# Optimization experiments

Measured on AMD Instinct MI355X. Metric: run time of the kernel, lower is better.

## Reference

```python
import jax, jax.numpy as jnp
import numpy as np

N_HEADS = 8
D_EMBED = 512
D_HEAD = D_EMBED // N_HEADS


def setup_inputs() -> dict:
    key = jax.random.key(0)
    ks = jax.random.split(key, 5)
    x = jax.random.normal(ks[0], (1, 4096, D_EMBED), dtype=jnp.float32)
    # in_proj: Linear(d, 3d); out_proj: Linear(d, d). Stored as [in, out] for x @ W.
    scale_in = 1.0 / np.sqrt(D_EMBED)
    W_in = jax.random.uniform(ks[1], (D_EMBED, 3 * D_EMBED), jnp.float32, -scale_in, scale_in)
    b_in = jax.random.uniform(ks[2], (3 * D_EMBED,), jnp.float32, -scale_in, scale_in)
    W_out = jax.random.uniform(ks[3], (D_EMBED, D_EMBED), jnp.float32, -scale_in, scale_in)
    b_out = jax.random.uniform(ks[4], (D_EMBED,), jnp.float32, -scale_in, scale_in)
    return {"x": x, "W_in": W_in, "b_in": b_in, "W_out": W_out, "b_out": b_out,
            "causal_mask": 1}


def reference(x, W_in, b_in, W_out, b_out, causal_mask):
    B, S, D = x.shape
    qkv = x @ W_in + b_in                      # [B, S, 3D]
    q, k, v = jnp.split(qkv, 3, axis=-1)
    # [B, S, D] -> [B, H, S, d_head]
    def split_heads(t):
        return t.reshape(B, S, N_HEADS, D_HEAD).transpose(0, 2, 1, 3)
    q, k, v = split_heads(q), split_heads(k), split_heads(v)
    weight = jnp.einsum("bhqd,bhkd->bhqk", q, k)  # [B, H, S, S]
    if causal_mask:
        mask = jnp.triu(jnp.ones((S, S), dtype=bool), k=1)
        weight = jnp.where(mask, -jnp.inf, weight)
    weight = weight / jnp.sqrt(jnp.float32(D_HEAD)).astype(weight.dtype)
    weight = jax.nn.softmax(weight, axis=-1)
    out = jnp.einsum("bhqk,bhkd->bhqd", weight, v)  # [B, H, S, d_head]
    out = out.transpose(0, 2, 1, 3).reshape(B, S, D)
    return out @ W_out + b_out
```

## Files before the change

### kernel.cpp

```cpp
#include <hip/hip_runtime.h>
#include <math.h>

#define SEQ 4096
#define DM 512
#define NH 8
#define DH 64
#define TQK (3 * DM)
#define QSCALE 0.18033688011112042f

typedef __attribute__((ext_vector_type(8))) short bf16x8;
typedef __attribute__((ext_vector_type(4))) float floatx4;
typedef unsigned short ushort_t;

__device__ __forceinline__ floatx4 mfma16(bf16x8 a, bf16x8 b, floatx4 c) {
    return __builtin_amdgcn_mfma_f32_16x16x32_bf16(a, b, c, 0, 0, 0);
}
__device__ __forceinline__ float ex2(float x) { return __builtin_amdgcn_exp2f(x); }

__device__ __forceinline__ unsigned int pk2(float a, float b) {
    unsigned int ua = __float_as_uint(a); ua = (ua + 0x7FFFu + ((ua >> 16) & 1u)) >> 16;
    unsigned int ub = __float_as_uint(b); ub = (ub + 0x7FFFu + ((ub >> 16) & 1u)) >> 16;
    return ua | (ub << 16);
}
__device__ __forceinline__ unsigned short f2bf(float x) {
    unsigned int u = __float_as_uint(x);
    return (unsigned short)((u + 0x7FFFu + ((u >> 16) & 1u)) >> 16);
}
__device__ __forceinline__ float bflo(unsigned int u) { return __uint_as_float(u << 16); }
__device__ __forceinline__ float bfhi(unsigned int u) { return __uint_as_float(u & 0xFFFF0000u); }

__device__ __forceinline__ void gload_lds16(const void* g, void* l) {
    __builtin_amdgcn_global_load_lds(
        (const __attribute__((address_space(1))) unsigned int*)g,
        (__attribute__((address_space(3))) unsigned int*)l, 16, 0, 0);
}

#define DPPMAX(x, ctrl) \
    (x) = fmaxf((x), __int_as_float(__builtin_amdgcn_update_dpp(0, __float_as_int(x), (ctrl), 0xF, 0xF, true)))
__device__ __forceinline__ float row_max16(float x) {
    DPPMAX(x, 0xB1);
    DPPMAX(x, 0x4E);
    DPPMAX(x, 0x141);
    DPPMAX(x, 0x140);
    return x;
}

__global__ __launch_bounds__(256) void prep(const float* __restrict__ x,
                                            const float* __restrict__ W_in,
                                            const float* __restrict__ W_out,
                                            ushort_t* __restrict__ xb,
                                            ushort_t* __restrict__ wti,
                                            ushort_t* __restrict__ wto) {
    __shared__ float T[64][65];
    const int bid = blockIdx.x, tid = threadIdx.x;
    if (bid < 1024) {
        const int i = bid * 256 + tid;
        const float4* p = (const float4*)x + (size_t)i * 2;
        float4 f0 = p[0], f1 = p[1];
        ((uint4*)xb)[i] = make_uint4(pk2(f0.x, f0.y), pk2(f0.z, f0.w),
                                     pk2(f1.x, f1.y), pk2(f1.z, f1.w));
        return;
    }
    const float* W; ushort_t* WT; int N, K, n0, k0; bool qscale;
    if (bid < 1216) { int id = bid - 1024; W = W_in;  WT = wti; N = TQK; K = DM;
                      n0 = (id % 24) * 64; k0 = (id / 24) * 64; qscale = true; }
    else            { int id = bid - 1216; W = W_out; WT = wto; N = DM;  K = DM;
                      n0 = (id % 8) * 64;  k0 = (id / 8) * 64;  qscale = false; }
    {
        const int r = tid >> 2, g = tid & 3;
        const float* src = W + (size_t)(k0 + r) * N + n0 + g * 16;
#pragma unroll
        for (int i = 0; i < 4; i++) {
            float4 f = ((const float4*)src)[i];
            T[g * 16 + i * 4 + 0][r] = f.x;
            T[g * 16 + i * 4 + 1][r] = f.y;
            T[g * 16 + i * 4 + 2][r] = f.z;
            T[g * 16 + i * 4 + 3][r] = f.w;
        }
    }
    __syncthreads();
    const int nr = tid >> 2, g2 = tid & 3;
    const float sc = (qscale && (n0 + nr < DM)) ? QSCALE : 1.0f;
    unsigned int pk[8];
#pragma unroll
    for (int j = 0; j < 8; j++)
        pk[j] = pk2(T[nr][g2 * 16 + 2 * j] * sc, T[nr][g2 * 16 + 2 * j + 1] * sc);
    ushort_t* dst = WT + (size_t)(n0 + nr) * K + k0 + g2 * 16;
    ((uint4*)dst)[0] = make_uint4(pk[0], pk[1], pk[2], pk[3]);
    ((uint4*)dst)[1] = make_uint4(pk[4], pk[5], pk[6], pk[7]);
}

__global__ __launch_bounds__(256) void gemm_in(const ushort_t* __restrict__ A,
                                               const ushort_t* __restrict__ BT,
                                               const float* __restrict__ bias,
                                               ushort_t* __restrict__ Cv,
                                               ushort_t* __restrict__ vt_out) {
    __shared__ __align__(16) ushort_t As[2][128 * 64];
    __shared__ __align__(16) ushort_t Bs[2][128 * 64];
    const int tid  = threadIdx.x;
    const int lane = tid & 63;
    const int w    = tid >> 6;
    const int quad = lane >> 4;
    const int ln   = lane & 15;
    const int row0 = blockIdx.y * 128;
    const int col0 = blockIdx.x * 128;
    const int wm = w >> 1, wn = w & 1;
    const int srow = lane >> 3;
    const int js   = (lane & 7) ^ srow;
    const int K = DM, N = TQK;

    floatx4 acc[4][4];
#pragma unroll
    for (int i = 0; i < 4; i++)
#pragma unroll
        for (int j = 0; j < 4; j++) acc[i][j] = (floatx4){0.f, 0.f, 0.f, 0.f};

#pragma unroll
    for (int i = 0; i < 4; i++) {
        const int c = w * 4 + i;
        gload_lds16(A  + (size_t)(row0 + c * 8 + srow) * K + js * 8, &As[0][c * 512]);
        gload_lds16(BT + (size_t)(col0 + c * 8 + srow) * K + js * 8, &Bs[0][c * 512]);
    }

    for (int kt = 0; kt < 8; kt++) {
        const int cur = kt & 1;
        __syncthreads();
        if (kt < 7) {
            const int k0n = (kt + 1) << 6;
#pragma unroll
            for (int i = 0; i < 4; i++) {
                const int c = w * 4 + i;
                gload_lds16(A  + (size_t)(row0 + c * 8 + srow) * K + k0n + js * 8, &As[cur ^ 1][c * 512]);
                gload_lds16(BT + (size_t)(col0 + c * 8 + srow) * K + k0n + js * 8, &Bs[cur ^ 1][c * 512]);
            }
        }
#pragma unroll
        for (int s = 0; s < 2; s++) {
            bf16x8 af[4], bfr[4];
#pragma unroll
            for (int i = 0; i < 4; i++) {
                const int lm = wm * 64 + i * 16 + ln;
                af[i] = *(const bf16x8*)&As[cur][lm * 64 + ((s * 4 + quad) ^ (ln & 7)) * 8];
                const int lnn = wn * 64 + i * 16 + ln;
                bfr[i] = *(const bf16x8*)&Bs[cur][lnn * 64 + ((s * 4 + quad) ^ (ln & 7)) * 8];
            }
#pragma unroll
            for (int i = 0; i < 4; i++)
#pragma unroll
                for (int j = 0; j < 4; j++)
                    acc[i][j] = mfma16(af[i], bfr[j], acc[i][j]);
        }
    }

    if (col0 >= 2 * DM) {
#pragma unroll
        for (int j = 0; j < 4; j++) {
            const int n = col0 + wn * 64 + j * 16 + ln;
            const float bv = bias[n];
#pragma unroll
            for (int i = 0; i < 4; i++) {
                const int mb = row0 + wm * 64 + i * 16 + quad * 4;
                uint2 pkd;
                pkd.x = pk2(acc[i][j][0] + bv, acc[i][j][1] + bv);
                pkd.y = pk2(acc[i][j][2] + bv, acc[i][j][3] + bv);
                *(uint2*)&vt_out[(size_t)(n - 2 * DM) * SEQ + mb] = pkd;
            }
        }
        return;
    }

#pragma unroll
    for (int j = 0; j < 4; j++) {
        const int n = col0 + wn * 64 + j * 16 + ln;
        const float bv = bias[n] * ((n < DM) ? QSCALE : 1.0f);
#pragma unroll
        for (int i = 0; i < 4; i++) {
            const int mb = row0 + wm * 64 + i * 16 + quad * 4;
#pragma unroll
            for (int r = 0; r < 4; r++)
                Cv[(size_t)(mb + r) * N + n] = f2bf(acc[i][j][r] + bv);
        }
    }
}

__global__ __launch_bounds__(256, 3) void attn_split(const ushort_t* __restrict__ qkv_b,
                                                     const ushort_t* __restrict__ vt,
                                                     ushort_t* __restrict__ po,
                                                     float2* __restrict__ pml) {
    __shared__ __align__(16) ushort_t Ks[2][64 * 64];
    __shared__ __align__(16) ushort_t Vs[2][64 * 64];
    __shared__ __align__(16) ushort_t Ps[128 * 72];

    const int tid  = threadIdx.x;
    const int lane = tid & 63;
    const int w    = tid >> 6;
    const int quad = lane >> 4;
    const int ln   = lane & 15;
    const int h    = blockIdx.y;
    const int lnx7 = ln & 7;

    const int e = 143 - (int)blockIdx.x;
    int g = 0;
    while (e >= 2 * (g + 1) * (g + 2)) g++;
    const int off = e - 2 * g * (g + 1);
    const int nc  = g + 1;
    const int qt  = 4 * g + off / nc;
    const int c   = off % nc;
    const int T   = 2 * qt + 2;
    const int jt0 = (c * T) / nc;
    const int jt1 = ((c + 1) * T) / nc;
    const int q0  = qt * 128;

    bf16x8 a0[2], a1[2];
#pragma unroll
    for (int qg = 0; qg < 2; qg++) {
        const ushort_t* qrow = qkv_b + (size_t)(q0 + w * 32 + qg * 16 + ln) * TQK + h * DH;
        a0[qg] = *(const bf16x8*)(qrow + quad * 8);
        a1[qg] = *(const bf16x8*)(qrow + quad * 8 + 32);
    }

    const short oneb = (short)0x3F80;
    const bf16x8 vone = {oneb, oneb, oneb, oneb, oneb, oneb, oneb, oneb};

    float m_q[2] = {-INFINITY, -INFINITY};
    floatx4 o[2][4], ol[2];
#pragma unroll
    for (int qg = 0; qg < 2; qg++) {
#pragma unroll
        for (int t = 0; t < 4; t++) o[qg][t] = (floatx4){0.f, 0.f, 0.f, 0.f};
        ol[qg] = (floatx4){0.f, 0.f, 0.f, 0.f};
    }

    const int srow = lane >> 3;
    const int js   = (lane & 7) ^ srow;

    {
        const int k0 = jt0 * 64;
#pragma unroll
        for (int i = 0; i < 2; i++) {
            const int cg = w * 2 + i;
            gload_lds16(qkv_b + (size_t)(k0 + cg * 8 + srow) * TQK + DM + h * DH + js * 8,
                        &Ks[0][cg * 512]);
            gload_lds16(vt + (size_t)(h * DH + cg * 8 + srow) * SEQ + k0 + js * 8,
                        &Vs[0][cg * 512]);
        }
    }

    for (int jt = jt0; jt < jt1; ++jt) {
        const int cur = (jt - jt0) & 1;
        const int k0  = jt * 64;
        __syncthreads();
        if (jt + 1 < jt1) {
            const int k0n = (jt + 1) * 64;
#pragma unroll
            for (int i = 0; i < 2; i++) {
                const int cg = w * 2 + i;
                gload_lds16(qkv_b + (size_t)(k0n + cg * 8 + srow) * TQK + DM + h * DH + js * 8,
                            &Ks[cur ^ 1][cg * 512]);
                gload_lds16(vt + (size_t)(h * DH + cg * 8 + srow) * SEQ + k0n + js * 8,
                            &Vs[cur ^ 1][cg * 512]);
            }
        }

        bf16x8 kb0[4], kb1[4];
#pragma unroll
        for (int t = 0; t < 4; t++) {
            const int n = t * 16 + ln;
            kb0[t] = *(const bf16x8*)&Ks[cur][n * 64 + ((quad) ^ lnx7) * 8];
            kb1[t] = *(const bf16x8*)&Ks[cur][n * 64 + ((4 + quad) ^ lnx7) * 8];
        }

#pragma unroll
        for (int qg = 0; qg < 2; qg++) {
            floatx4 sa[4];
#pragma unroll
            for (int t = 0; t < 4; t++) {
                floatx4 acc = {0.f, 0.f, 0.f, 0.f};
                acc = mfma16(a0[qg], kb0[t], acc);
                acc = mfma16(a1[qg], kb1[t], acc);
                sa[t] = acc;
            }

            if (k0 + 63 > q0 + w * 32 + qg * 16) {
#pragma unroll
                for (int t = 0; t < 4; t++) {
                    const int cg2 = k0 + t * 16 + ln;
#pragma unroll
                    for (int r = 0; r < 4; r++) {
                        const int rg = q0 + w * 32 + qg * 16 + quad * 4 + r;
                        if (cg2 > rg) sa[t][r] = -INFINITY;
                    }
                }
            }

            float mx = sa[0][0];
#pragma unroll
            for (int t = 0; t < 4; t++)
#pragma unroll
                for (int r = 0; r < 4; r++) mx = fmaxf(mx, sa[t][r]);
            mx = row_max16(mx);
            const float mn = fmaxf(fmaxf(m_q[qg], mx), -1e30f);
            const float alpha = ex2(m_q[qg] - mn);
            m_q[qg] = mn;
#pragma unroll
            for (int t = 0; t < 4; t++)
#pragma unroll
                for (int r = 0; r < 4; r++) {
                    const float p = ex2(sa[t][r] - mn);
                    Ps[(w * 32 + qg * 16 + quad * 4 + r) * 72 + t * 16 + ln] =
                        (ushort_t)(__float_as_uint(p) >> 16);
                }
            if (alpha < 1.0f) {
#pragma unroll
                for (int t = 0; t < 4; t++)
#pragma unroll
                    for (int r = 0; r < 4; r++) o[qg][t][r] *= alpha;
#pragma unroll
                for (int r = 0; r < 4; r++) ol[qg][r] *= alpha;
            }
        }

        __builtin_amdgcn_wave_barrier();

#pragma unroll
        for (int t = 0; t < 4; t++) {
            const int d = t * 16 + ln;
            const bf16x8 v0 = *(const bf16x8*)&Vs[cur][d * 64 + ((quad) ^ lnx7) * 8];
            const bf16x8 v1 = *(const bf16x8*)&Vs[cur][d * 64 + ((4 + quad) ^ lnx7) * 8];
#pragma unroll
            for (int qg = 0; qg < 2; qg++) {
                const bf16x8 p0 = *(const bf16x8*)&Ps[(w * 32 + qg * 16 + ln) * 72 + quad * 8];
                const bf16x8 p1 = *(const bf16x8*)&Ps[(w * 32 + qg * 16 + ln) * 72 + quad * 8 + 32];
                o[qg][t] = mfma16(p0, v0, o[qg][t]);
                o[qg][t] = mfma16(p1, v1, o[qg][t]);
                if (t == 0) {
                    ol[qg] = mfma16(p0, vone, ol[qg]);
                    ol[qg] = mfma16(p1, vone, ol[qg]);
                }
            }
        }
    }

    const size_t pbase  = ((size_t)h * 144 + e) * (128 * 64);
    const size_t mlbase = ((size_t)h * 144 + e) * 128;
#pragma unroll
    for (int qg = 0; qg < 2; qg++) {
#pragma unroll
        for (int t = 0; t < 4; t++)
#pragma unroll
            for (int r = 0; r < 4; r++)
                po[pbase + (size_t)(w * 32 + qg * 16 + quad * 4 + r) * 64 + t * 16 + ln] =
                    f2bf(o[qg][t][r]);
        if (ln == 0) {
#pragma unroll
            for (int r = 0; r < 4; r++)
                pml[mlbase + w * 32 + qg * 16 + quad * 4 + r] = make_float2(m_q[qg], ol[qg][r]);
        }
    }
}

__global__ __launch_bounds__(512) void attn_combine(const ushort_t* __restrict__ po,
                                                    const float2* __restrict__ pml,
                                                    ushort_t* __restrict__ aob) {
    const int qt = blockIdx.x, h = blockIdx.y;
    const int gq = qt >> 2;
    const int nc = gq + 1;
    const int sbase = 2 * gq * (gq + 1) + (qt & 3) * nc;
    const int row = threadIdx.x >> 2, g = threadIdx.x & 3;

    float2 ml[8];
    float M = -INFINITY;
    for (int ci = 0; ci < nc; ci++) {
        ml[ci] = pml[((size_t)h * 144 + sbase + ci) * 128 + row];
        M = fmaxf(M, ml[ci].x);
    }
    float L = 0.f;
    float acc[16];
#pragma unroll
    for (int j = 0; j < 16; j++) acc[j] = 0.f;

    for (int ci = 0; ci < nc; ci++) {
        const float wgt = ex2(ml[ci].x - M);
        L += wgt * ml[ci].y;
        const ushort_t* p = po + ((size_t)h * 144 + sbase + ci) * (128 * 64)
                               + (size_t)row * 64 + g * 16;
        uint4 u0 = ((const uint4*)p)[0];
        uint4 u1 = ((const uint4*)p)[1];
        const unsigned int uu[8] = {u0.x, u0.y, u0.z, u0.w, u1.x, u1.y, u1.z, u1.w};
#pragma unroll
        for (int j = 0; j < 8; j++) {
            acc[2 * j]     += wgt * bflo(uu[j]);
            acc[2 * j + 1] += wgt * bfhi(uu[j]);
        }
    }
    const float inv = 1.0f / L;
    unsigned int pk[8];
#pragma unroll
    for (int j = 0; j < 8; j++)
        pk[j] = pk2(acc[2 * j] * inv, acc[2 * j + 1] * inv);
    ushort_t* dst = aob + (size_t)(qt * 128 + row) * DM + h * DH + g * 16;
    ((uint4*)dst)[0] = make_uint4(pk[0], pk[1], pk[2], pk[3]);
    ((uint4*)dst)[1] = make_uint4(pk[4], pk[5], pk[6], pk[7]);
}

__global__ __launch_bounds__(256) void gemm_out(const ushort_t* __restrict__ A,
                                                const ushort_t* __restrict__ BT,
                                                const float* __restrict__ bias,
                                                float* __restrict__ out) {
    __shared__ __align__(16) ushort_t As[2][128 * 64];
    __shared__ __align__(16) ushort_t Bs[2][64 * 64];
    const int tid  = threadIdx.x;
    const int lane = tid & 63;
    const int w    = tid >> 6;
    const int quad = lane >> 4;
    const int ln   = lane & 15;
    const int row0 = blockIdx.y * 128;
    const int col0 = blockIdx.x * 64;
    const int wm = w >> 1, wn = w & 1;
    const int srow = lane >> 3;
    const int js   = (lane & 7) ^ srow;

    floatx4 acc[4][2];
#pragma unroll
    for (int i = 0; i < 4; i++)
#pragma unroll
        for (int j = 0; j < 2; j++) acc[i][j] = (floatx4){0.f, 0.f, 0.f, 0.f};

#pragma unroll
    for (int i = 0; i < 4; i++) {
        const int c = w * 4 + i;
        gload_lds16(A + (size_t)(row0 + c * 8 + srow) * DM + js * 8, &As[0][c * 512]);
    }
#pragma unroll
    for (int i = 0; i < 2; i++) {
        const int c = w * 2 + i;
        gload_lds16(BT + (size_t)(col0 + c * 8 + srow) * DM + js * 8, &Bs[0][c * 512]);
    }

    for (int kt = 0; kt < 8; kt++) {
        const int cur = kt & 1;
        __syncthreads();
        if (kt < 7) {
            const int k0n = (kt + 1) << 6;
#pragma unroll
            for (int i = 0; i < 4; i++) {
                const int c = w * 4 + i;
                gload_lds16(A + (size_t)(row0 + c * 8 + srow) * DM + k0n + js * 8, &As[cur ^ 1][c * 512]);
            }
#pragma unroll
            for (int i = 0; i < 2; i++) {
                const int c = w * 2 + i;
                gload_lds16(BT + (size_t)(col0 + c * 8 + srow) * DM + k0n + js * 8, &Bs[cur ^ 1][c * 512]);
            }
        }
#pragma unroll
        for (int s = 0; s < 2; s++) {
            bf16x8 af[4], bfr[2];
#pragma unroll
            for (int i = 0; i < 4; i++) {
                const int lm = wm * 64 + i * 16 + ln;
                af[i] = *(const bf16x8*)&As[cur][lm * 64 + ((s * 4 + quad) ^ (ln & 7)) * 8];
            }
#pragma unroll
            for (int j = 0; j < 2; j++) {
                const int lnn = wn * 32 + j * 16 + ln;
                bfr[j] = *(const bf16x8*)&Bs[cur][lnn * 64 + ((s * 4 + quad) ^ (ln & 7)) * 8];
            }
#pragma unroll
            for (int i = 0; i < 4; i++)
#pragma unroll
                for (int j = 0; j < 2; j++)
                    acc[i][j] = mfma16(af[i], bfr[j], acc[i][j]);
        }
    }

#pragma unroll
    for (int j = 0; j < 2; j++) {
        const int n = col0 + wn * 32 + j * 16 + ln;
        const float bv = bias[n];
#pragma unroll
        for (int i = 0; i < 4; i++) {
            const int mb = row0 + wm * 64 + i * 16 + quad * 4;
#pragma unroll
            for (int r = 0; r < 4; r++)
                out[(size_t)(mb + r) * DM + n] = acc[i][j][r] + bv;
        }
    }
}

extern "C" void kernel_launch(void* const* d_in, const int* in_sizes, int n_in,
                              void* d_out, int out_size, void* d_ws, size_t ws_size,
                              hipStream_t stream) {
    const float* x     = (const float*)d_in[0];
    const float* W_in  = (const float*)d_in[1];
    const float* b_in  = (const float*)d_in[2];
    const float* W_out = (const float*)d_in[3];
    const float* b_out = (const float*)d_in[4];
    float* out = (float*)d_out;

    char* ws = (char*)d_ws;
    ushort_t* xb    = (ushort_t*)ws;
    ushort_t* wti   = (ushort_t*)(ws + (4u  << 20));
    ushort_t* wto   = (ushort_t*)(ws + (6u  << 20));
    ushort_t* qkv_b = (ushort_t*)(ws + (7u  << 20));
    ushort_t* vtb   = (ushort_t*)(ws + (19u << 20));
    ushort_t* po    = (ushort_t*)(ws + (23u << 20));
    float2*   pml   = (float2*)  (ws + (42u << 20));
    ushort_t* aob   = (ushort_t*)(ws + (44u << 20));

    prep<<<1280, 256, 0, stream>>>(x, W_in, W_out, xb, wti, wto);

    gemm_in<<<dim3(TQK / 128, SEQ / 128), 256, 0, stream>>>(xb, wti, b_in, qkv_b, vtb);

    attn_split<<<dim3(144, NH), 256, 0, stream>>>(qkv_b, vtb, po, pml);

    attn_combine<<<dim3(SEQ / 128, NH), 512, 0, stream>>>(po, pml, aob);

    gemm_out<<<dim3(DM / 64, SEQ / 128), 256, 0, stream>>>(aob, wto, b_out, out);
}
```

Before: 156.0 us.

## Load K/V directly from global memory and split attention into more chunks

Removes the double-buffered LDS staging of K and V tiles, along with the per-iteration block barrier. Each wave now reads its K and V fragments straight from global memory, relying on the cache for reuse across the four waves. The work split changes from 144 to 272 chunks per head, with (q/2)+1 chunks per query tile, and occupancy is raised to 4 blocks per CU. The intent is more parallelism and less sync and LDS pressure, in exchange for redundant global/L2 traffic per wave, larger partial buffers, and more combine work.

```diff
diff --git a/kernel.cpp b/kernel.cpp
--- a/kernel.cpp
+++ b/kernel.cpp
@@ -183,12 +183,10 @@
     }
 }
 
-__global__ __launch_bounds__(256, 3) void attn_split(const ushort_t* __restrict__ qkv_b,
+__global__ __launch_bounds__(256, 4) void attn_split(const ushort_t* __restrict__ qkv_b,
                                                      const ushort_t* __restrict__ vt,
                                                      ushort_t* __restrict__ po,
                                                      float2* __restrict__ pml) {
-    __shared__ __align__(16) ushort_t Ks[2][64 * 64];
-    __shared__ __align__(16) ushort_t Vs[2][64 * 64];
     __shared__ __align__(16) ushort_t Ps[128 * 72];
 
     const int tid  = threadIdx.x;
@@ -197,18 +195,20 @@
     const int quad = lane >> 4;
     const int ln   = lane & 15;
     const int h    = blockIdx.y;
-    const int lnx7 = ln & 7;
-
-    const int e = 143 - (int)blockIdx.x;
-    int g = 0;
-    while (e >= 2 * (g + 1) * (g + 2)) g++;
-    const int off = e - 2 * g * (g + 1);
-    const int nc  = g + 1;
-    const int qt  = 4 * g + off / nc;
-    const int c   = off % nc;
+
+    int qt = 0, nc = 1, cc = 0;
+    {
+        const int bx = blockIdx.x;
+        int acc = 0;
+        for (int q = 0; q < 32; q++) {
+            const int n = (q >> 1) + 1;
+            if (bx < acc + n) { qt = q; nc = n; cc = bx - acc; break; }
+            acc += n;
+        }
+    }
     const int T   = 2 * qt + 2;
-    const int jt0 = (c * T) / nc;
-    const int jt1 = ((c + 1) * T) / nc;
+    const int jt0 = (cc * T) / nc;
+    const int jt1 = ((cc + 1) * T) / nc;
     const int q0  = qt * 128;
 
     bf16x8 a0[2], a1[2];
@@ -231,56 +231,41 @@
         ol[qg] = (floatx4){0.f, 0.f, 0.f, 0.f};
     }
 
-    const int srow = lane >> 3;
-    const int js   = (lane & 7) ^ srow;
-
-    {
-        const int k0 = jt0 * 64;
-#pragma unroll
-        for (int i = 0; i < 2; i++) {
-            const int cg = w * 2 + i;
-            gload_lds16(qkv_b + (size_t)(k0 + cg * 8 + srow) * TQK + DM + h * DH + js * 8,
-                        &Ks[0][cg * 512]);
-            gload_lds16(vt + (size_t)(h * DH + cg * 8 + srow) * SEQ + k0 + js * 8,
-                        &Vs[0][cg * 512]);
-        }
-    }
+    const ushort_t* kbase = qkv_b + DM + h * DH;
+    const ushort_t* vbase = vt + (size_t)h * DH * SEQ;
 
     for (int jt = jt0; jt < jt1; ++jt) {
-        const int cur = (jt - jt0) & 1;
-        const int k0  = jt * 64;
-        __syncthreads();
-        if (jt + 1 < jt1) {
-            const int k0n = (jt + 1) * 64;
-#pragma unroll
-            for (int i = 0; i < 2; i++) {
-                const int cg = w * 2 + i;
-                gload_lds16(qkv_b + (size_t)(k0n + cg * 8 + srow) * TQK + DM + h * DH + js * 8,
-                            &Ks[cur ^ 1][cg * 512]);
-                gload_lds16(vt + (size_t)(h * DH + cg * 8 + srow) * SEQ + k0n + js * 8,
-                            &Vs[cur ^ 1][cg * 512]);
-            }
-        }
+        const int k0 = jt * 64;
 
         bf16x8 kb0[4], kb1[4];
 #pragma unroll
         for (int t = 0; t < 4; t++) {
-            const int n = t * 16 + ln;
-            kb0[t] = *(const bf16x8*)&Ks[cur][n * 64 + ((quad) ^ lnx7) * 8];
-            kb1[t] = *(const bf16x8*)&Ks[cur][n * 64 + ((4 + quad) ^ lnx7) * 8];
-        }
-
-#pragma unroll
-        for (int qg = 0; qg < 2; qg++) {
-            floatx4 sa[4];
+            const ushort_t* kr = kbase + (size_t)(k0 + t * 16 + ln) * TQK + quad * 8;
+            kb0[t] = *(const bf16x8*)kr;
+            kb1[t] = *(const bf16x8*)(kr + 32);
+        }
+
+        floatx4 sa[2][4];
+#pragma unroll
+        for (int qg = 0; qg < 2; qg++)
 #pragma unroll
             for (int t = 0; t < 4; t++) {
                 floatx4 acc = {0.f, 0.f, 0.f, 0.f};
                 acc = mfma16(a0[qg], kb0[t], acc);
                 acc = mfma16(a1[qg], kb1[t], acc);
-                sa[t] = acc;
-            }
-
+                sa[qg][t] = acc;
+            }
+
+        bf16x8 v0[4], v1[4];
+#pragma unroll
+        for (int t = 0; t < 4; t++) {
+            const ushort_t* vr = vbase + (size_t)(t * 16 + ln) * SEQ + k0 + quad * 8;
+            v0[t] = *(const bf16x8*)vr;
+            v1[t] = *(const bf16x8*)(vr + 32);
+        }
+
+#pragma unroll
+        for (int qg = 0; qg < 2; qg++) {
             if (k0 + 63 > q0 + w * 32 + qg * 16) {
 #pragma unroll
                 for (int t = 0; t < 4; t++) {
@@ -288,16 +273,16 @@
 #pragma unroll
                     for (int r = 0; r < 4; r++) {
                         const int rg = q0 + w * 32 + qg * 16 + quad * 4 + r;
-                        if (cg2 > rg) sa[t][r] = -INFINITY;
+                        if (cg2 > rg) sa[qg][t][r] = -INFINITY;
                     }
                 }
             }
 
-            float mx = sa[0][0];
+            float mx = sa[qg][0][0];
 #pragma unroll
             for (int t = 0; t < 4; t++)
 #pragma unroll
-                for (int r = 0; r < 4; r++) mx = fmaxf(mx, sa[t][r]);
+                for (int r = 0; r < 4; r++) mx = fmaxf(mx, sa[qg][t][r]);
             mx = row_max16(mx);
             const float mn = fmaxf(fmaxf(m_q[qg], mx), -1e30f);
             const float alpha = ex2(m_q[qg] - mn);
@@ -306,7 +291,7 @@
             for (int t = 0; t < 4; t++)
 #pragma unroll
                 for (int r = 0; r < 4; r++) {
-                    const float p = ex2(sa[t][r] - mn);
+                    const float p = ex2(sa[qg][t][r] - mn);
                     Ps[(w * 32 + qg * 16 + quad * 4 + r) * 72 + t * 16 + ln] =
                         (ushort_t)(__float_as_uint(p) >> 16);
                 }
@@ -323,26 +308,21 @@
         __builtin_amdgcn_wave_barrier();
 
 #pragma unroll
-        for (int t = 0; t < 4; t++) {
-            const int d = t * 16 + ln;
-            const bf16x8 v0 = *(const bf16x8*)&Vs[cur][d * 64 + ((quad) ^ lnx7) * 8];
-            const bf16x8 v1 = *(const bf16x8*)&Vs[cur][d * 64 + ((4 + quad) ^ lnx7) * 8];
-#pragma unroll
-            for (int qg = 0; qg < 2; qg++) {
-                const bf16x8 p0 = *(const bf16x8*)&Ps[(w * 32 + qg * 16 + ln) * 72 + quad * 8];
-                const bf16x8 p1 = *(const bf16x8*)&Ps[(w * 32 + qg * 16 + ln) * 72 + quad * 8 + 32];
-                o[qg][t] = mfma16(p0, v0, o[qg][t]);
-                o[qg][t] = mfma16(p1, v1, o[qg][t]);
-                if (t == 0) {
-                    ol[qg] = mfma16(p0, vone, ol[qg]);
-                    ol[qg] = mfma16(p1, vone, ol[qg]);
-                }
-            }
-        }
-    }
-
-    const size_t pbase  = ((size_t)h * 144 + e) * (128 * 64);
-    const size_t mlbase = ((size_t)h * 144 + e) * 128;
+        for (int qg = 0; qg < 2; qg++) {
+            const bf16x8 p0 = *(const bf16x8*)&Ps[(w * 32 + qg * 16 + ln) * 72 + quad * 8];
+            const bf16x8 p1 = *(const bf16x8*)&Ps[(w * 32 + qg * 16 + ln) * 72 + quad * 8 + 32];
+#pragma unroll
+            for (int t = 0; t < 4; t++) {
+                o[qg][t] = mfma16(p0, v0[t], o[qg][t]);
+                o[qg][t] = mfma16(p1, v1[t], o[qg][t]);
+            }
+            ol[qg] = mfma16(p0, vone, ol[qg]);
+            ol[qg] = mfma16(p1, vone, ol[qg]);
+        }
+    }
+
+    const size_t pbase  = ((size_t)h * 272 + blockIdx.x) * (128 * 64);
+    const size_t mlbase = ((size_t)h * 272 + blockIdx.x) * 128;
 #pragma unroll
     for (int qg = 0; qg < 2; qg++) {
 #pragma unroll
@@ -363,15 +343,15 @@
                                                     const float2* __restrict__ pml,
                                                     ushort_t* __restrict__ aob) {
     const int qt = blockIdx.x, h = blockIdx.y;
-    const int gq = qt >> 2;
-    const int nc = gq + 1;
-    const int sbase = 2 * gq * (gq + 1) + (qt & 3) * nc;
+    const int nc = (qt >> 1) + 1;
+    int sbase = 0;
+    for (int q = 0; q < qt; q++) sbase += (q >> 1) + 1;
     const int row = threadIdx.x >> 2, g = threadIdx.x & 3;
 
-    float2 ml[8];
+    float2 ml[16];
     float M = -INFINITY;
     for (int ci = 0; ci < nc; ci++) {
-        ml[ci] = pml[((size_t)h * 144 + sbase + ci) * 128 + row];
+        ml[ci] = pml[((size_t)h * 272 + sbase + ci) * 128 + row];
         M = fmaxf(M, ml[ci].x);
     }
     float L = 0.f;
@@ -382,7 +362,7 @@
     for (int ci = 0; ci < nc; ci++) {
         const float wgt = ex2(ml[ci].x - M);
         L += wgt * ml[ci].y;
-        const ushort_t* p = po + ((size_t)h * 144 + sbase + ci) * (128 * 64)
+        const ushort_t* p = po + ((size_t)h * 272 + sbase + ci) * (128 * 64)
                                + (size_t)row * 64 + g * 16;
         uint4 u0 = ((const uint4*)p)[0];
         uint4 u1 = ((const uint4*)p)[1];
@@ -505,14 +485,14 @@
     ushort_t* qkv_b = (ushort_t*)(ws + (7u  << 20));
     ushort_t* vtb   = (ushort_t*)(ws + (19u << 20));
     ushort_t* po    = (ushort_t*)(ws + (23u << 20));
-    float2*   pml   = (float2*)  (ws + (42u << 20));
-    ushort_t* aob   = (ushort_t*)(ws + (44u << 20));
+    float2*   pml   = (float2*)  (ws + (59u << 20));
+    ushort_t* aob   = (ushort_t*)(ws + (62u << 20));
 
     prep<<<1280, 256, 0, stream>>>(x, W_in, W_out, xb, wti, wto);
 
     gemm_in<<<dim3(TQK / 128, SEQ / 128), 256, 0, stream>>>(xb, wti, b_in, qkv_b, vtb);
 
-    attn_split<<<dim3(144, NH), 256, 0, stream>>>(qkv_b, vtb, po, pml);
+    attn_split<<<dim3(272, NH), 256, 0, stream>>>(qkv_b, vtb, po, pml);
 
     attn_combine<<<dim3(SEQ / 128, NH), 512, 0, stream>>>(po, pml, aob);
 
```

Measured after the change: 209.6 us. +34.3%, slower.
